# Kernel tuning notes

Measured on AMD Instinct MI355X. Metric: run time of the kernel, lower is better.

Reference implementation:

```python
import jax, jax.numpy as jnp
import numpy as np

B, N, D, H = 16, 1024, 384, 6
DH = D // H  # 64 per-head dim


def _layernorm(x, w, b, eps=1e-5):
    mu = jnp.mean(x, axis=-1, keepdims=True)
    var = jnp.var(x, axis=-1, keepdims=True)
    return (x - mu) * jax.lax.rsqrt(var + eps) * w + b


def setup_inputs() -> dict:
    key = jax.random.key(0)
    ks = jax.random.split(key, 10)
    std = 0.02
    return {
        "X": jax.random.normal(ks[0], (B, N, D), dtype=jnp.float32),
        "Wq": jax.random.normal(ks[1], (H, DH, D), dtype=jnp.float32) * std,
        "Wk": jax.random.normal(ks[2], (H, DH, D), dtype=jnp.float32) * std,
        "Wv": jax.random.normal(ks[3], (H, DH, D), dtype=jnp.float32) * std,
        "Wo": jax.random.normal(ks[4], (D, D), dtype=jnp.float32) * std,
        "bo": jnp.zeros((D,), dtype=jnp.float32),
        "ln1_w": jnp.ones((D,), dtype=jnp.float32),
        "ln1_b": jnp.zeros((D,), dtype=jnp.float32),
        "ln2_w": jnp.ones((D,), dtype=jnp.float32),
        "ln2_b": jnp.zeros((D,), dtype=jnp.float32),
        "W1": jax.random.normal(ks[5], (2 * D, D), dtype=jnp.float32) * std,
        "b1": jnp.zeros((2 * D,), dtype=jnp.float32),
        "W2": jax.random.normal(ks[6], (D, 2 * D), dtype=jnp.float32) * std,
        "b2": jnp.zeros((D,), dtype=jnp.float32),
    }


def reference(X, Wq, Wk, Wv, Wo, bo, ln1_w, ln1_b, ln2_w, ln2_b, W1, b1, W2, b2):
    scale = 1.0 / jnp.sqrt(jnp.float32(DH))
    # pre-LN then multi-head attention (heads vectorized, math identical to per-head loop)
    t = _layernorm(X, ln1_w, ln1_b)                       # [B,N,D]
    q = jnp.einsum('bnd,hkd->bhnk', t, Wq)                # [B,H,N,DH]
    k = jnp.einsum('bnd,hkd->bhnk', t, Wk)
    v = jnp.einsum('bnd,hkd->bhnk', t, Wv)
    scores = jnp.einsum('bhnk,bhmk->bhnm', q, k) * scale  # [B,H,N,N]
    p = jax.nn.softmax(scores, axis=-1)
    o = jnp.einsum('bhnm,bhmk->bhnk', p, v)               # [B,H,N,DH]
    o = jnp.transpose(o, (0, 2, 1, 3)).reshape(B, N, D)   # concat heads
    attn = o @ Wo.T + bo
    # residual + post-LN (dropout/drop_path are identity in eval)
    X2 = _layernorm(X + attn, ln2_w, ln2_b)
    # MLP: Linear -> exact GELU -> Linear
    h = jax.nn.gelu(X2 @ W1.T + b1, approximate=False)
    mlp = h @ W2.T + b2
    return X2 + mlp
```

## Files before the change

### kernel.cpp

```cpp
#include <hip/hip_runtime.h>
#include <math.h>

typedef float  f32x4  __attribute__((ext_vector_type(4)));
typedef __bf16 bf16x8 __attribute__((ext_vector_type(8)));
typedef __bf16 bf16x4 __attribute__((ext_vector_type(4)));

__device__ __forceinline__ void gload16(const void* g, void* l) {
  __builtin_amdgcn_global_load_lds((__attribute__((address_space(1))) const void*)g,
                                   (__attribute__((address_space(3))) void*)l, 16, 0, 0);
}

__device__ __forceinline__ f32x4 mfma16(bf16x8 a, bf16x8 b, f32x4 c) {
  return __builtin_amdgcn_mfma_f32_16x16x32_bf16(a, b, c, 0, 0, 0);
}

__device__ __forceinline__ float fast_gelu(float x) {
  const float xs = x * 0.70710678118654752f;
  const float ax = fabsf(xs);
  const float t  = __builtin_amdgcn_rcpf(1.f + 0.3275911f * ax);
  const float poly = ((((1.061405429f*t - 1.453152027f)*t + 1.421413741f)*t
                       - 0.284496736f)*t + 0.254829592f)*t;
  const float e = __builtin_amdgcn_exp2f(-1.4426950408889634f * ax * ax);
  float erfv = 1.f - poly * e;
  erfv = (xs < 0.f) ? -erfv : erfv;
  return 0.5f * x * (1.f + erfv);
}

__global__ __launch_bounds__(256) void prep_kernel(
    const float* __restrict__ X, const float* __restrict__ ln1w, const float* __restrict__ ln1b,
    __bf16* __restrict__ t_bf,
    const float* __restrict__ Wq, const float* __restrict__ Wk, const float* __restrict__ Wv,
    const float* __restrict__ Wo, const float* __restrict__ W1, const float* __restrict__ W2,
    __bf16* __restrict__ wqkv, __bf16* __restrict__ wo, __bf16* __restrict__ w1, __bf16* __restrict__ w2)
{
  if (blockIdx.x >= 4096) {
    const int idx = ((blockIdx.x - 4096) * 256 + threadIdx.x) * 4;
    const float* src; __bf16* dst; int off;
    if      (idx < 147456) { src = Wq; dst = wqkv;          off = idx; }
    else if (idx < 294912) { src = Wk; dst = wqkv + 147456; off = idx - 147456; }
    else if (idx < 442368) { src = Wv; dst = wqkv + 294912; off = idx - 294912; }
    else if (idx < 589824) { src = Wo; dst = wo;            off = idx - 442368; }
    else if (idx < 884736) { src = W1; dst = w1;            off = idx - 589824; }
    else                   { src = W2; dst = w2;            off = idx - 884736; }
    f32x4 v = *(const f32x4*)(src + off);
    bf16x4 o = {(__bf16)v.x, (__bf16)v.y, (__bf16)v.z, (__bf16)v.w};
    *(bf16x4*)(dst + off) = o;
    return;
  }
  const int row  = blockIdx.x * 4 + (threadIdx.x >> 6);
  const int lane = threadIdx.x & 63;
  const float* x = X + (size_t)row * 384;
  float v[6]; float s = 0.f;
#pragma unroll
  for (int j = 0; j < 6; ++j) { v[j] = x[lane + 64*j]; s += v[j]; }
#pragma unroll
  for (int off = 32; off > 0; off >>= 1) s += __shfl_xor(s, off);
  const float mu = s * (1.f/384.f);
  float s2 = 0.f;
#pragma unroll
  for (int j = 0; j < 6; ++j) { float d = v[j] - mu; s2 += d*d; }
#pragma unroll
  for (int off = 32; off > 0; off >>= 1) s2 += __shfl_xor(s2, off);
  const float inv = rsqrtf(s2 * (1.f/384.f) + 1e-5f);
#pragma unroll
  for (int j = 0; j < 6; ++j) {
    const int cidx = lane + 64*j;
    t_bf[(size_t)row*384 + cidx] = (__bf16)((v[j]-mu)*inv*ln1w[cidx] + ln1b[cidx]);
  }
}

__global__ __launch_bounds__(256) void ln_kernel(
    const float* __restrict__ in, const float* __restrict__ w, const float* __restrict__ b,
    __bf16* __restrict__ outb, float* __restrict__ outf)
{
  const int row  = blockIdx.x * 4 + (threadIdx.x >> 6);
  const int lane = threadIdx.x & 63;
  const float* x = in + (size_t)row * 384;
  float v[6]; float s = 0.f;
#pragma unroll
  for (int j = 0; j < 6; ++j) { v[j] = x[lane + 64*j]; s += v[j]; }
#pragma unroll
  for (int off = 32; off > 0; off >>= 1) s += __shfl_xor(s, off);
  const float mu = s * (1.f/384.f);
  float s2 = 0.f;
#pragma unroll
  for (int j = 0; j < 6; ++j) { float d = v[j] - mu; s2 += d*d; }
#pragma unroll
  for (int off = 32; off > 0; off >>= 1) s2 += __shfl_xor(s2, off);
  const float inv = rsqrtf(s2 * (1.f/384.f) + 1e-5f);
#pragma unroll
  for (int j = 0; j < 6; ++j) {
    const int cidx = lane + 64*j;
    const float y = (v[j]-mu)*inv*w[cidx] + b[cidx];
    outb[(size_t)row*384 + cidx] = (__bf16)y;
    outf[(size_t)row*384 + cidx] = y;
  }
}

template<int EPI>
__global__ __launch_bounds__(256, 3) void gemm_bt(
    const __bf16* __restrict__ A, const __bf16* __restrict__ Bw,
    int N, int K,
    const float* __restrict__ bias, const float* __restrict__ resid,
    float* __restrict__ outf, __bf16* __restrict__ outb,
    __bf16* __restrict__ q_out, __bf16* __restrict__ k_out, __bf16* __restrict__ vt_out)
{
  __shared__ __attribute__((aligned(16))) __bf16 As[2][4096];
  __shared__ __attribute__((aligned(16))) __bf16 Bs[2][4096];
  const int tid  = threadIdx.x;
  const int lane = tid & 63;
  const int w    = tid >> 6;
  const int wm   = w >> 1, wn = w & 1;
  const int m0   = blockIdx.x * 128, n0 = blockIdx.y * 128;

  f32x4 acc[4][4] = {};

  const int srow = lane & 15, skq = lane >> 4;
  const __bf16* gptr[4];
  __bf16*       lptr[4];
#pragma unroll
  for (int r = 0; r < 4; ++r) {
    const int id = r * 4 + w;
    if (id < 8) {
      gptr[r] = A + (size_t)(m0 + id*16 + srow) * K + (skq << 3);
      lptr[r] = &As[0][id * 512];
    } else {
      const int j = id - 8;
      gptr[r] = Bw + (size_t)(n0 + j*16 + srow) * K + (skq << 3);
      lptr[r] = &Bs[0][j * 512];
    }
  }

  auto stage = [&](int kk, int b) {
#pragma unroll
    for (int r = 0; r < 4; ++r)
      gload16(gptr[r] + kk * 32, lptr[r] + b * 4096);
  };
  auto compute = [&](int b) {
    bf16x8 af[4], bfr[4];
#pragma unroll
    for (int i = 0; i < 4; ++i)
      af[i] = *(const bf16x8*)&As[b][(wm*4 + i) * 512 + lane * 8];
#pragma unroll
    for (int j = 0; j < 4; ++j)
      bfr[j] = *(const bf16x8*)&Bs[b][(wn*4 + j) * 512 + lane * 8];
#pragma unroll
    for (int i = 0; i < 4; ++i)
#pragma unroll
      for (int j = 0; j < 4; ++j)
        acc[i][j] = mfma16(af[i], bfr[j], acc[i][j]);
  };

  const int NIT = K >> 5;
  stage(0, 0);
  __syncthreads();
  for (int k = 0; k < NIT; ++k) {
    const int b = k & 1;
    if (k + 1 < NIT) stage(k + 1, b ^ 1);
    compute(b);
    __syncthreads();
  }

  const int quad = lane >> 4, cc = lane & 15;
#pragma unroll
  for (int rt = 0; rt < 4; ++rt) {
#pragma unroll
    for (int ct = 0; ct < 4; ++ct) {
      const int gr0 = m0 + (wm*4 + rt)*16 + quad*4;
      const int gc  = n0 + (wn*4 + ct)*16 + cc;
      f32x4 a = acc[rt][ct];
      if constexpr (EPI == 0) {
        const int bb = gr0 >> 10, nn = gr0 & 1023;
        if (gc >= 768) {
          const int jj = gc - 768, hh = jj >> 6, dh = jj & 63;
          bf16x4 pk = {(__bf16)a[0], (__bf16)a[1], (__bf16)a[2], (__bf16)a[3]};
          *(bf16x4*)&vt_out[((size_t)((bb*6 + hh)*64 + dh) << 10) + nn] = pk;
        } else {
          const bool isq = (gc < 384);
          const int jj = isq ? gc : (gc - 384);
          __bf16* dst = isq ? q_out : k_out;
          const float sc = isq ? 0.18033688011112042f : 1.0f;
          const int hh = jj >> 6, dh = jj & 63;
#pragma unroll
          for (int i = 0; i < 4; ++i)
            dst[((size_t)(((bb*6 + hh) << 10) | (nn + i)) << 6) + dh] = (__bf16)(a[i] * sc);
        }
      } else {
#pragma unroll
        for (int i = 0; i < 4; ++i) {
          const int gr = gr0 + i;
          float val = a[i];
          if constexpr (EPI == 1) {
            const size_t idx = (size_t)gr * N + gc;
            outf[idx] = val + bias[gc] + resid[idx];
          } else if constexpr (EPI == 2) {
            outb[(size_t)gr * N + gc] = (__bf16)fast_gelu(val + bias[gc]);
          } else {
            const size_t idx = (size_t)gr * N + gc;
            outf[idx] = outf[idx] + val + bias[gc];
          }
        }
      }
    }
  }
}

__global__ __launch_bounds__(256, 3) void attn_kernel(
    const __bf16* __restrict__ qp, const __bf16* __restrict__ kp,
    const __bf16* __restrict__ vtp, __bf16* __restrict__ omat)
{
  __shared__ __attribute__((aligned(16))) __bf16 Ks[2][4096];
  __shared__ __attribute__((aligned(16))) __bf16 Vs[2][4096];
  __shared__ __attribute__((aligned(16))) __bf16 Ps[4][2][1088];
  const int tid = threadIdx.x, lane = tid & 63, w = tid >> 6;
  const int bh = blockIdx.x;
  const int q0 = blockIdx.y * 128 + w * 32;
  const int quad = lane >> 4, lo = lane & 15;

  bf16x8 qa[2][2];
#pragma unroll
  for (int t = 0; t < 2; ++t) {
    const __bf16* qb = qp + ((size_t)bh * 1024 + q0 + t*16 + lo) * 64 + (quad << 3);
    qa[t][0] = *(const bf16x8*)qb;
    qa[t][1] = *(const bf16x8*)(qb + 32);
  }

  f32x4 oacc[2][4] = {};
  float l_r[2] = {0.f, 0.f};

  auto stage = [&](int c, int bb) {
#pragma unroll
    for (int s = 0; s < 2; ++s) {
      const int ck = s * 256 + tid;
      const int l = ck & 63, g = ck >> 6;
      const int ct = g >> 1, ks = g & 1;
      const __bf16* gk = kp + ((size_t)bh*1024 + c*64 + ct*16 + (l & 15)) * 64
                            + ks*32 + ((l >> 4) << 3);
      gload16(gk, &Ks[bb][(ck & ~63) * 8]);
      const __bf16* gv = vtp + (((size_t)(bh*64 + ct*16 + (l & 15))) << 10)
                             + c*64 + ks*32 + ((l >> 4) << 3);
      gload16(gv, &Vs[bb][(ck & ~63) * 8]);
    }
  };

  stage(0, 0);
  __syncthreads();

  for (int c = 0; c < 16; ++c) {
    const int bb = c & 1;
    if (c + 1 < 16) stage(c + 1, bb ^ 1);

    f32x4 st[2][4];
#pragma unroll
    for (int ct = 0; ct < 4; ++ct) {
      bf16x8 kb0 = *(const bf16x8*)&Ks[bb][((ct*2 + 0)*64 + lane) * 8];
      bf16x8 kb1 = *(const bf16x8*)&Ks[bb][((ct*2 + 1)*64 + lane) * 8];
#pragma unroll
      for (int t = 0; t < 2; ++t) {
        f32x4 s0 = {};
        s0 = mfma16(kb0, qa[t][0], s0);
        s0 = mfma16(kb1, qa[t][1], s0);
        st[t][ct] = s0;
      }
    }
#pragma unroll
    for (int t = 0; t < 2; ++t)
#pragma unroll
      for (int ct = 0; ct < 4; ++ct) {
        const float p0 = __builtin_amdgcn_exp2f(st[t][ct][0]);
        const float p1 = __builtin_amdgcn_exp2f(st[t][ct][1]);
        const float p2 = __builtin_amdgcn_exp2f(st[t][ct][2]);
        const float p3 = __builtin_amdgcn_exp2f(st[t][ct][3]);
        l_r[t] += (p0 + p1) + (p2 + p3);
        bf16x4 pk = {(__bf16)p0, (__bf16)p1, (__bf16)p2, (__bf16)p3};
        *(bf16x4*)&Ps[w][t][lo*68 + ct*16 + quad*4] = pk;
      }
    bf16x8 pa[2][2];
#pragma unroll
    for (int t = 0; t < 2; ++t)
#pragma unroll
      for (int ks = 0; ks < 2; ++ks)
        pa[t][ks] = *(const bf16x8*)&Ps[w][t][lo*68 + ks*32 + (quad << 3)];
#pragma unroll
    for (int dt = 0; dt < 4; ++dt)
#pragma unroll
      for (int ks = 0; ks < 2; ++ks) {
        bf16x8 vb = *(const bf16x8*)&Vs[bb][((dt*2 + ks)*64 + lane) * 8];
#pragma unroll
        for (int t = 0; t < 2; ++t)
          oacc[t][dt] = mfma16(pa[t][ks], vb, oacc[t][dt]);
      }
    __syncthreads();
  }

  const int b = bh / 6, h = bh - (bh / 6) * 6;
#pragma unroll
  for (int t = 0; t < 2; ++t) {
    float ls = l_r[t];
    ls += __shfl_xor(ls, 16);
    ls += __shfl_xor(ls, 32);
#pragma unroll
    for (int i = 0; i < 4; ++i) {
      const float linv = 1.f / __shfl(ls, quad*4 + i);
      const int n = q0 + t*16 + quad*4 + i;
#pragma unroll
      for (int dt = 0; dt < 4; ++dt)
        omat[((size_t)((b << 10) | n)) * 384 + (h << 6) + dt*16 + lo] =
            (__bf16)(oacc[t][dt][i] * linv);
    }
  }
}

extern "C" void kernel_launch(void* const* d_in, const int* in_sizes, int n_in,
                              void* d_out, int out_size, void* d_ws, size_t ws_size,
                              hipStream_t stream)
{
  const float* X    = (const float*)d_in[0];
  const float* Wq   = (const float*)d_in[1];
  const float* Wk   = (const float*)d_in[2];
  const float* Wv   = (const float*)d_in[3];
  const float* Wo   = (const float*)d_in[4];
  const float* bo   = (const float*)d_in[5];
  const float* ln1w = (const float*)d_in[6];
  const float* ln1b = (const float*)d_in[7];
  const float* ln2w = (const float*)d_in[8];
  const float* ln2b = (const float*)d_in[9];
  const float* W1   = (const float*)d_in[10];
  const float* b1   = (const float*)d_in[11];
  const float* W2   = (const float*)d_in[12];
  const float* b2   = (const float*)d_in[13];

  char* ws = (char*)d_ws;
  __bf16* t_bf  = (__bf16*)(ws + 0);
  __bf16* q_bf  = (__bf16*)(ws + 12582912);
  __bf16* k_bf  = (__bf16*)(ws + 25165824);
  __bf16* omat  = (__bf16*)(ws + 37748736);
  __bf16* vt_bf = (__bf16*)(ws + 50331648);
  float*  s1    = (float*) (ws + 62914560);
  __bf16* h_bf  = (__bf16*)(ws + 62914560);
  __bf16* wqkv  = (__bf16*)(ws + 88080384);
  __bf16* wo_b  = (__bf16*)(ws + 88965120);
  __bf16* w1_b  = (__bf16*)(ws + 89260032);
  __bf16* w2_b  = (__bf16*)(ws + 89849856);
  __bf16* x2_bf = t_bf;
  float*  out   = (float*)d_out;

  prep_kernel<<<5248, 256, 0, stream>>>(X, ln1w, ln1b, t_bf,
      Wq, Wk, Wv, Wo, W1, W2, wqkv, wo_b, w1_b, w2_b);
  gemm_bt<0><<<dim3(128,9), 256, 0, stream>>>(t_bf, wqkv, 1152, 384,
      nullptr, nullptr, nullptr, nullptr, q_bf, k_bf, vt_bf);
  attn_kernel<<<dim3(96,8), 256, 0, stream>>>(q_bf, k_bf, vt_bf, omat);
  gemm_bt<1><<<dim3(128,3), 256, 0, stream>>>(omat, wo_b, 384, 384,
      bo, X, s1, nullptr, nullptr, nullptr, nullptr);
  ln_kernel<<<4096, 256, 0, stream>>>(s1, ln2w, ln2b, x2_bf, out);
  gemm_bt<2><<<dim3(128,6), 256, 0, stream>>>(x2_bf, w1_b, 768, 384,
      b1, nullptr, nullptr, h_bf, nullptr, nullptr, nullptr);
  gemm_bt<3><<<dim3(128,3), 256, 0, stream>>>(h_bf, w2_b, 384, 768,
      b2, nullptr, out, nullptr, nullptr, nullptr, nullptr);
}
```

Baseline: 270.9 us.

## Enlarge attention query tile, add 256-row QKV GEMM variant, split-K final GEMM

Each attention wave now handles 64 query rows instead of 32, so every staged K/V chunk is reused across twice as many queries. The launch bound drops to 2 blocks per CU to make room for the extra registers. The GEMM is templated on M-warps: the QKV projection uses 512-thread blocks covering 256 rows, which reuses each weight tile more. The final MLP GEMM is split along K into two slices that accumulate into the output with atomicAdd, doubling its block count at the cost of atomic traffic and a nondeterministic summation order.

```diff
diff --git a/kernel.cpp b/kernel.cpp
--- a/kernel.cpp
+++ b/kernel.cpp
@@ -97,44 +97,51 @@
   }
 }
 
-template<int EPI>
-__global__ __launch_bounds__(256, 3) void gemm_bt(
+template<int EPI, int MW>
+__global__ __launch_bounds__(MW * 128, MW == 4 ? 6 : 3) void gemm_bt(
     const __bf16* __restrict__ A, const __bf16* __restrict__ Bw,
-    int N, int K,
+    int N, int Kstr, int KSL,
     const float* __restrict__ bias, const float* __restrict__ resid,
     float* __restrict__ outf, __bf16* __restrict__ outb,
     __bf16* __restrict__ q_out, __bf16* __restrict__ k_out, __bf16* __restrict__ vt_out)
 {
-  __shared__ __attribute__((aligned(16))) __bf16 As[2][4096];
+  constexpr int NW   = 2 * MW;
+  constexpr int ASUB = MW * 4;
+  constexpr int P    = (ASUB + 8) / NW;
+  __shared__ __attribute__((aligned(16))) __bf16 As[2][ASUB * 512];
   __shared__ __attribute__((aligned(16))) __bf16 Bs[2][4096];
   const int tid  = threadIdx.x;
   const int lane = tid & 63;
   const int w    = tid >> 6;
   const int wm   = w >> 1, wn = w & 1;
-  const int m0   = blockIdx.x * 128, n0 = blockIdx.y * 128;
+  const int m0   = blockIdx.x * (MW * 64), n0 = blockIdx.y * 128;
+  const int kofs = blockIdx.z * KSL;
 
   f32x4 acc[4][4] = {};
 
   const int srow = lane & 15, skq = lane >> 4;
-  const __bf16* gptr[4];
-  __bf16*       lptr[4];
-#pragma unroll
-  for (int r = 0; r < 4; ++r) {
-    const int id = r * 4 + w;
-    if (id < 8) {
-      gptr[r] = A + (size_t)(m0 + id*16 + srow) * K + (skq << 3);
+  const __bf16* gptr[P];
+  __bf16*       lptr[P];
+  int           lstr[P];
+#pragma unroll
+  for (int r = 0; r < P; ++r) {
+    const int id = r * NW + w;
+    if (id < ASUB) {
+      gptr[r] = A + (size_t)(m0 + id*16 + srow) * Kstr + kofs + (skq << 3);
       lptr[r] = &As[0][id * 512];
+      lstr[r] = ASUB * 512;
     } else {
-      const int j = id - 8;
-      gptr[r] = Bw + (size_t)(n0 + j*16 + srow) * K + (skq << 3);
+      const int j = id - ASUB;
+      gptr[r] = Bw + (size_t)(n0 + j*16 + srow) * Kstr + kofs + (skq << 3);
       lptr[r] = &Bs[0][j * 512];
+      lstr[r] = 4096;
     }
   }
 
   auto stage = [&](int kk, int b) {
 #pragma unroll
-    for (int r = 0; r < 4; ++r)
-      gload16(gptr[r] + kk * 32, lptr[r] + b * 4096);
+    for (int r = 0; r < P; ++r)
+      gload16(gptr[r] + kk * 32, lptr[r] + b * lstr[r]);
   };
   auto compute = [&](int b) {
     bf16x8 af[4], bfr[4];
@@ -151,7 +158,7 @@
         acc[i][j] = mfma16(af[i], bfr[j], acc[i][j]);
   };
 
-  const int NIT = K >> 5;
+  const int NIT = KSL >> 5;
   stage(0, 0);
   __syncthreads();
   for (int k = 0; k < NIT; ++k) {
@@ -197,7 +204,8 @@
             outb[(size_t)gr * N + gc] = (__bf16)fast_gelu(val + bias[gc]);
           } else {
             const size_t idx = (size_t)gr * N + gc;
-            outf[idx] = outf[idx] + val + bias[gc];
+            const float bb2 = (blockIdx.z == 0) ? bias[gc] : 0.f;
+            atomicAdd(&outf[idx], val + bb2);
           }
         }
       }
@@ -205,28 +213,28 @@
   }
 }
 
-__global__ __launch_bounds__(256, 3) void attn_kernel(
+__global__ __launch_bounds__(256, 2) void attn_kernel(
     const __bf16* __restrict__ qp, const __bf16* __restrict__ kp,
     const __bf16* __restrict__ vtp, __bf16* __restrict__ omat)
 {
   __shared__ __attribute__((aligned(16))) __bf16 Ks[2][4096];
   __shared__ __attribute__((aligned(16))) __bf16 Vs[2][4096];
-  __shared__ __attribute__((aligned(16))) __bf16 Ps[4][2][1088];
+  __shared__ __attribute__((aligned(16))) __bf16 Ps[4][4][1088];
   const int tid = threadIdx.x, lane = tid & 63, w = tid >> 6;
   const int bh = blockIdx.x;
-  const int q0 = blockIdx.y * 128 + w * 32;
+  const int q0 = blockIdx.y * 256 + w * 64;
   const int quad = lane >> 4, lo = lane & 15;
 
-  bf16x8 qa[2][2];
-#pragma unroll
-  for (int t = 0; t < 2; ++t) {
+  bf16x8 qa[4][2];
+#pragma unroll
+  for (int t = 0; t < 4; ++t) {
     const __bf16* qb = qp + ((size_t)bh * 1024 + q0 + t*16 + lo) * 64 + (quad << 3);
     qa[t][0] = *(const bf16x8*)qb;
     qa[t][1] = *(const bf16x8*)(qb + 32);
   }
 
-  f32x4 oacc[2][4] = {};
-  float l_r[2] = {0.f, 0.f};
+  f32x4 oacc[4][4] = {};
+  float l_r[4] = {0.f, 0.f, 0.f, 0.f};
 
   auto stage = [&](int c, int bb) {
 #pragma unroll
@@ -250,13 +258,13 @@
     const int bb = c & 1;
     if (c + 1 < 16) stage(c + 1, bb ^ 1);
 
-    f32x4 st[2][4];
+    f32x4 st[4][4];
 #pragma unroll
     for (int ct = 0; ct < 4; ++ct) {
       bf16x8 kb0 = *(const bf16x8*)&Ks[bb][((ct*2 + 0)*64 + lane) * 8];
       bf16x8 kb1 = *(const bf16x8*)&Ks[bb][((ct*2 + 1)*64 + lane) * 8];
 #pragma unroll
-      for (int t = 0; t < 2; ++t) {
+      for (int t = 0; t < 4; ++t) {
         f32x4 s0 = {};
         s0 = mfma16(kb0, qa[t][0], s0);
         s0 = mfma16(kb1, qa[t][1], s0);
@@ -264,7 +272,7 @@
       }
     }
 #pragma unroll
-    for (int t = 0; t < 2; ++t)
+    for (int t = 0; t < 4; ++t)
 #pragma unroll
       for (int ct = 0; ct < 4; ++ct) {
         const float p0 = __builtin_amdgcn_exp2f(st[t][ct][0]);
@@ -275,9 +283,9 @@
         bf16x4 pk = {(__bf16)p0, (__bf16)p1, (__bf16)p2, (__bf16)p3};
         *(bf16x4*)&Ps[w][t][lo*68 + ct*16 + quad*4] = pk;
       }
-    bf16x8 pa[2][2];
-#pragma unroll
-    for (int t = 0; t < 2; ++t)
+    bf16x8 pa[4][2];
+#pragma unroll
+    for (int t = 0; t < 4; ++t)
 #pragma unroll
       for (int ks = 0; ks < 2; ++ks)
         pa[t][ks] = *(const bf16x8*)&Ps[w][t][lo*68 + ks*32 + (quad << 3)];
@@ -287,7 +295,7 @@
       for (int ks = 0; ks < 2; ++ks) {
         bf16x8 vb = *(const bf16x8*)&Vs[bb][((dt*2 + ks)*64 + lane) * 8];
 #pragma unroll
-        for (int t = 0; t < 2; ++t)
+        for (int t = 0; t < 4; ++t)
           oacc[t][dt] = mfma16(pa[t][ks], vb, oacc[t][dt]);
       }
     __syncthreads();
@@ -295,7 +303,7 @@
 
   const int b = bh / 6, h = bh - (bh / 6) * 6;
 #pragma unroll
-  for (int t = 0; t < 2; ++t) {
+  for (int t = 0; t < 4; ++t) {
     float ls = l_r[t];
     ls += __shfl_xor(ls, 16);
     ls += __shfl_xor(ls, 32);
@@ -347,14 +355,14 @@
 
   prep_kernel<<<5248, 256, 0, stream>>>(X, ln1w, ln1b, t_bf,
       Wq, Wk, Wv, Wo, W1, W2, wqkv, wo_b, w1_b, w2_b);
-  gemm_bt<0><<<dim3(128,9), 256, 0, stream>>>(t_bf, wqkv, 1152, 384,
+  gemm_bt<0,4><<<dim3(64,9), 512, 0, stream>>>(t_bf, wqkv, 1152, 384, 384,
       nullptr, nullptr, nullptr, nullptr, q_bf, k_bf, vt_bf);
-  attn_kernel<<<dim3(96,8), 256, 0, stream>>>(q_bf, k_bf, vt_bf, omat);
-  gemm_bt<1><<<dim3(128,3), 256, 0, stream>>>(omat, wo_b, 384, 384,
+  attn_kernel<<<dim3(96,4), 256, 0, stream>>>(q_bf, k_bf, vt_bf, omat);
+  gemm_bt<1,2><<<dim3(128,3), 256, 0, stream>>>(omat, wo_b, 384, 384, 384,
       bo, X, s1, nullptr, nullptr, nullptr, nullptr);
   ln_kernel<<<4096, 256, 0, stream>>>(s1, ln2w, ln2b, x2_bf, out);
-  gemm_bt<2><<<dim3(128,6), 256, 0, stream>>>(x2_bf, w1_b, 768, 384,
+  gemm_bt<2,2><<<dim3(128,6), 256, 0, stream>>>(x2_bf, w1_b, 768, 384, 384,
       b1, nullptr, nullptr, h_bf, nullptr, nullptr, nullptr);
-  gemm_bt<3><<<dim3(128,3), 256, 0, stream>>>(h_bf, w2_b, 384, 768,
+  gemm_bt<3,2><<<dim3(128,3,2), 256, 0, stream>>>(h_bf, w2_b, 384, 768, 384,
       b2, nullptr, out, nullptr, nullptr, nullptr, nullptr);
 }
```

Result: slower. 399.1 us (+47.3%).
